# Kernel tuning notes

Hardware: AMD Instinct MI355X
Metric: run time of the kernel (lower is better)

The kernel has to match this reference:

```python
import jax, jax.numpy as jnp
from jax import lax
import numpy as np

SEQ_LEN, BATCH, INPUT_SIZE, HIDDEN_SIZE = 1024, 64, 512, 512


def setup_inputs() -> dict:
    key = jax.random.key(0)
    k1, k2, k3 = jax.random.split(key, 3)
    inputs = jax.random.normal(k1, (SEQ_LEN, BATCH, INPUT_SIZE), dtype=jnp.float32)
    # nn.Linear(input_size + hidden_size, hidden_size): W [H, I+H], b [H]
    fan_in = INPUT_SIZE + HIDDEN_SIZE
    bound = 1.0 / np.sqrt(fan_in)
    W = jax.random.uniform(k2, (HIDDEN_SIZE, fan_in), minval=-bound, maxval=bound, dtype=jnp.float32)
    b = jax.random.uniform(k3, (HIDDEN_SIZE,), minval=-bound, maxval=bound, dtype=jnp.float32)
    return {"inputs": inputs, "W": W, "b": b}


def reference(inputs, W, b):
    # inputs: [T, B, I]; hidden starts at zeros [B, H]
    hidden_size = W.shape[0]
    # Split W into hidden part and input part to avoid per-step concat:
    # layer_input = cat(h, x) -> y = h @ Wh^T + x @ Wx^T + b
    Wh = W[:, :hidden_size]          # [H, H]
    Wx = W[:, hidden_size:]          # [H, I]
    h0 = jnp.zeros((inputs.shape[1], hidden_size), dtype=inputs.dtype)

    def step(h, x):
        h_new = jnp.tanh(h @ Wh.T + x @ Wx.T + b)
        return h_new, None

    h_final, _ = lax.scan(step, h0, inputs)
    return h_final
```

## Files before the change

### kernel.cpp

```cpp
#include <hip/hip_runtime.h>


#define SEQ 1024
#define NB  64
#define HID 512

typedef _Float16 half2v __attribute__((ext_vector_type(2)));
typedef _Float16 f16x8  __attribute__((ext_vector_type(8)));
typedef float    f32x4  __attribute__((ext_vector_type(4)));

#if __has_builtin(__builtin_amdgcn_fdot2)
#define DOT2(a, b, c) __builtin_amdgcn_fdot2((a), (b), (c), false)
#else
static __device__ __forceinline__ float DOT2(half2v a, half2v b, float c) {
  return c + (float)a.x * (float)b.x + (float)a.y * (float)b.y;
}
#endif

static __device__ __forceinline__ float fast_tanh(float x) {
  float e = __expf(2.0f * x);
  return (e - 1.0f) / (e + 1.0f);
}

__global__ __launch_bounds__(256, 2)
void rnn_prepass(const float* __restrict__ X, const float* __restrict__ W,
                 const float* __restrict__ bias, _Float16* __restrict__ U) {
  __shared__ __align__(16) _Float16 As[128][40];
  __shared__ __align__(16) _Float16 Bs[128][40];
  const int tid = threadIdx.x;
  const int m0 = blockIdx.x * 128;
  const int n0 = blockIdx.y * 128;
  const int wave = tid >> 6, lane = tid & 63;
  const int wm = (wave >> 1) * 64, wn = (wave & 1) * 64;
  const int l15 = lane & 15, q = lane >> 4;

  f32x4 acc[4][4];
#pragma unroll
  for (int i = 0; i < 4; ++i)
#pragma unroll
    for (int j = 0; j < 4; ++j) acc[i][j] = (f32x4){0.f, 0.f, 0.f, 0.f};

  const int srow = tid >> 1;
  const int shalf = (tid & 1) * 16;

  for (int k0 = 0; k0 < 512; k0 += 32) {
    const float* asrc = X + (size_t)(m0 + srow) * 512 + k0 + shalf;
    const float* bsrc = W + (size_t)(n0 + srow) * 1024 + 512 + k0 + shalf;
    float4 a0 = *(const float4*)(asrc);
    float4 a1 = *(const float4*)(asrc + 4);
    float4 a2 = *(const float4*)(asrc + 8);
    float4 a3 = *(const float4*)(asrc + 12);
    float4 b0 = *(const float4*)(bsrc);
    float4 b1 = *(const float4*)(bsrc + 4);
    float4 b2 = *(const float4*)(bsrc + 8);
    float4 b3 = *(const float4*)(bsrc + 12);
    __syncthreads();
    f16x8 pa0 = {(_Float16)a0.x, (_Float16)a0.y, (_Float16)a0.z, (_Float16)a0.w,
                 (_Float16)a1.x, (_Float16)a1.y, (_Float16)a1.z, (_Float16)a1.w};
    f16x8 pa1 = {(_Float16)a2.x, (_Float16)a2.y, (_Float16)a2.z, (_Float16)a2.w,
                 (_Float16)a3.x, (_Float16)a3.y, (_Float16)a3.z, (_Float16)a3.w};
    f16x8 pb0 = {(_Float16)b0.x, (_Float16)b0.y, (_Float16)b0.z, (_Float16)b0.w,
                 (_Float16)b1.x, (_Float16)b1.y, (_Float16)b1.z, (_Float16)b1.w};
    f16x8 pb1 = {(_Float16)b2.x, (_Float16)b2.y, (_Float16)b2.z, (_Float16)b2.w,
                 (_Float16)b3.x, (_Float16)b3.y, (_Float16)b3.z, (_Float16)b3.w};
    *(f16x8*)&As[srow][shalf] = pa0;
    *(f16x8*)&As[srow][shalf + 8] = pa1;
    *(f16x8*)&Bs[srow][shalf] = pb0;
    *(f16x8*)&Bs[srow][shalf + 8] = pb1;
    __syncthreads();
    f16x8 av[4], bv[4];
#pragma unroll
    for (int i = 0; i < 4; ++i)
      av[i] = *(const f16x8*)&As[wm + i * 16 + l15][q * 8];
#pragma unroll
    for (int j = 0; j < 4; ++j)
      bv[j] = *(const f16x8*)&Bs[wn + j * 16 + l15][q * 8];
#pragma unroll
    for (int i = 0; i < 4; ++i)
#pragma unroll
      for (int j = 0; j < 4; ++j)
        acc[i][j] = __builtin_amdgcn_mfma_f32_16x16x32_f16(av[i], bv[j], acc[i][j], 0, 0, 0);
  }
  float bj[4];
#pragma unroll
  for (int j = 0; j < 4; ++j) bj[j] = bias[n0 + wn + j * 16 + l15];
#pragma unroll
  for (int i = 0; i < 4; ++i)
#pragma unroll
    for (int j = 0; j < 4; ++j)
#pragma unroll
      for (int r = 0; r < 4; ++r) {
        int m = m0 + wm + i * 16 + q * 4 + r;
        int n = n0 + wn + j * 16 + l15;
        U[(size_t)m * 512 + n] = (_Float16)(acc[i][j][r] + bj[j]);
      }
}

__global__ __launch_bounds__(256, 1)
void rnn_recur(const float* __restrict__ W, const _Float16* __restrict__ U,
               unsigned long long* hbuf, float* __restrict__ out) {
  const int blk = blockIdx.x;
  const int batch = blk & 63;
  const int g = blk >> 6;
  const int tid = threadIdx.x;
  const int rg = tid & 31;
  const int c = tid >> 5;

  __shared__ __align__(16) f16x8 wlds[32][256];
  __shared__ half2v hlds[256];
  __shared__ float part[128][9];

  {
#pragma unroll
    for (int i = 0; i < 4; ++i) {
      const float* wrow = W + (size_t)(128 * g + rg * 4 + i) * 1024 + c * 64;
#pragma unroll
      for (int qq = 0; qq < 8; ++qq) {
        float4 wa = *(const float4*)(wrow + 8 * qq);
        float4 wb = *(const float4*)(wrow + 8 * qq + 4);
        f16x8 p = {(_Float16)wa.x, (_Float16)wa.y, (_Float16)wa.z, (_Float16)wa.w,
                   (_Float16)wb.x, (_Float16)wb.y, (_Float16)wb.z, (_Float16)wb.w};
        wlds[i * 8 + qq][tid] = p;
      }
    }
  }
  __syncthreads();

  const unsigned int* ubase = (const unsigned int*)U;
  unsigned long long* hb = hbuf + (size_t)batch * 256;
  unsigned long long* hpub = hb + (size_t)(NB * 256) * 0;

  float h0f = 0.f, h1f = 0.f;
  for (int t = 0; t < SEQ; ++t) {
    unsigned int ubits = 0;
    if (tid < 64)
      ubits = ubase[((size_t)t * NB + batch) * 256 + g * 64 + tid];

    {
      const unsigned long long* src =
          hb + (size_t)(t & 1) * (NB * 256) + tid;
      unsigned long long e;
      do {
        e = __hip_atomic_load(src, __ATOMIC_RELAXED, __HIP_MEMORY_SCOPE_AGENT);
      } while ((unsigned int)(e >> 32) != (unsigned int)t);
      hlds[tid] = __builtin_bit_cast(half2v, (unsigned int)e);
    }
    __syncthreads();

    float a0 = 0.f, a1 = 0.f, a2 = 0.f, a3 = 0.f;
    const half2v* hp = &hlds[c * 32];
#pragma unroll
    for (int qq = 0; qq < 8; ++qq) {
      half2v hv0 = hp[qq * 4 + 0];
      half2v hv1 = hp[qq * 4 + 1];
      half2v hv2 = hp[qq * 4 + 2];
      half2v hv3 = hp[qq * 4 + 3];
#pragma unroll
      for (int i = 0; i < 4; ++i) {
        f16x8 wv = wlds[i * 8 + qq][tid];
        half2v w0 = {wv[0], wv[1]};
        half2v w1 = {wv[2], wv[3]};
        half2v w2 = {wv[4], wv[5]};
        half2v w3 = {wv[6], wv[7]};
        float* ai = (i == 0) ? &a0 : (i == 1) ? &a1 : (i == 2) ? &a2 : &a3;
        *ai = DOT2(w0, hv0, *ai);
        *ai = DOT2(w1, hv1, *ai);
        *ai = DOT2(w2, hv2, *ai);
        *ai = DOT2(w3, hv3, *ai);
      }
    }
    part[rg * 4 + 0][c] = a0;
    part[rg * 4 + 1][c] = a1;
    part[rg * 4 + 2][c] = a2;
    part[rg * 4 + 3][c] = a3;
    __syncthreads();

    if (tid < 64) {
      float s0 = 0.f, s1 = 0.f;
#pragma unroll
      for (int cc = 0; cc < 8; ++cc) {
        s0 += part[2 * tid][cc];
        s1 += part[2 * tid + 1][cc];
      }
      half2v uh = __builtin_bit_cast(half2v, ubits);
      h0f = fast_tanh(s0 + (float)uh.x);
      h1f = fast_tanh(s1 + (float)uh.y);
      half2v hh;
      hh.x = (_Float16)h0f;
      hh.y = (_Float16)h1f;
      unsigned long long word =
          ((unsigned long long)(unsigned int)(t + 1) << 32) |
          (unsigned long long)__builtin_bit_cast(unsigned int, hh);
      __hip_atomic_store(
          hb + (size_t)((t + 1) & 1) * (NB * 256) + g * 64 + tid, word,
          __ATOMIC_RELAXED, __HIP_MEMORY_SCOPE_AGENT);
    }
  }
  if (tid < 64) {
    out[(size_t)batch * HID + 128 * g + 2 * tid] = h0f;
    out[(size_t)batch * HID + 128 * g + 2 * tid + 1] = h1f;
  }
  (void)hpub;
}

extern "C" void kernel_launch(void* const* d_in, const int* in_sizes, int n_in,
                              void* d_out, int out_size, void* d_ws, size_t ws_size,
                              hipStream_t stream) {
  const float* X    = (const float*)d_in[0];
  const float* W    = (const float*)d_in[1];
  const float* bias = (const float*)d_in[2];
  float* out = (float*)d_out;

  char* ws = (char*)d_ws;
  _Float16* U = (_Float16*)ws;
  unsigned long long* hbuf =
      (unsigned long long*)(ws + (size_t)SEQ * NB * HID * 2);

  hipMemsetAsync(hbuf, 0, (size_t)NB * 256 * 8, stream);

  rnn_prepass<<<dim3(512, 4), dim3(256), 0, stream>>>(X, W, bias, U);

  const float* Wp = W;
  const _Float16* Up = U;
  unsigned long long* hb = hbuf;
  float* op = out;
  void* args[] = {(void*)&Wp, (void*)&Up, (void*)&hb, (void*)&op};
  hipError_t e = hipLaunchCooperativeKernel(
      reinterpret_cast<void*>(rnn_recur), dim3(256), dim3(256), args, 0, stream);
  if (e != hipSuccess) {
    rnn_recur<<<dim3(256), dim3(256), 0, stream>>>(Wp, Up, hb, op);
  }
}
```

Baseline: 1.586 ms.

## Repartition recurrent blocks to two batches by sixty-four hidden rows

The recurrent kernel now gives each block two batch rows and a 64-row slice of the hidden weight, instead of one batch and a 128-row slice. Each weight value loaded from LDS is reused for two batch columns, which halves the per-block weight LDS footprint and the weight reads per FMA. The cost is that each block must poll and load the full hidden state of two batches every step. Each step now depends on 16 producer blocks instead of 4, which can lengthen the per-step synchronisation latency.

```diff
diff --git a/kernel.cpp b/kernel.cpp
--- a/kernel.cpp
+++ b/kernel.cpp
@@ -100,87 +100,98 @@
 void rnn_recur(const float* __restrict__ W, const _Float16* __restrict__ U,
                unsigned long long* hbuf, float* __restrict__ out) {
   const int blk = blockIdx.x;
-  const int batch = blk & 63;
-  const int g = blk >> 6;
+  const int p = blk & 31;
+  const int g = blk >> 5;
   const int tid = threadIdx.x;
-  const int rg = tid & 31;
-  const int c = tid >> 5;
-
-  __shared__ __align__(16) f16x8 wlds[32][256];
-  __shared__ half2v hlds[256];
-  __shared__ float part[128][9];
-
-  {
-#pragma unroll
-    for (int i = 0; i < 4; ++i) {
-      const float* wrow = W + (size_t)(128 * g + rg * 4 + i) * 1024 + c * 64;
-#pragma unroll
-      for (int qq = 0; qq < 8; ++qq) {
-        float4 wa = *(const float4*)(wrow + 8 * qq);
-        float4 wb = *(const float4*)(wrow + 8 * qq + 4);
-        f16x8 p = {(_Float16)wa.x, (_Float16)wa.y, (_Float16)wa.z, (_Float16)wa.w,
-                   (_Float16)wb.x, (_Float16)wb.y, (_Float16)wb.z, (_Float16)wb.w};
-        wlds[i * 8 + qq][tid] = p;
-      }
-    }
-  }
-  __syncthreads();
-
-  const unsigned int* ubase = (const unsigned int*)U;
-  unsigned long long* hb = hbuf + (size_t)batch * 256;
-  unsigned long long* hpub = hb + (size_t)(NB * 256) * 0;
+  const int rb = tid & 15;
+  const int kc = tid >> 4;
+
+  __shared__ __align__(16) f16x8 wlds[16][256];
+  __shared__ __align__(16) half2v hlds[2][256];
+  __shared__ float part[128][33];
+
+#pragma unroll
+  for (int i = 0; i < 4; ++i) {
+    const float* wrow = W + (size_t)(64 * g + rb * 4 + i) * 1024 + kc * 32;
+#pragma unroll
+    for (int q = 0; q < 4; ++q) {
+      float4 wa = *(const float4*)(wrow + 8 * q);
+      float4 wb = *(const float4*)(wrow + 8 * q + 4);
+      f16x8 pk = {(_Float16)wa.x, (_Float16)wa.y, (_Float16)wa.z, (_Float16)wa.w,
+                  (_Float16)wb.x, (_Float16)wb.y, (_Float16)wb.z, (_Float16)wb.w};
+      wlds[i * 4 + q][tid] = pk;
+    }
+  }
+
+  const unsigned int* U32 = (const unsigned int*)U;
+  const int rr = tid & 31, bb = tid >> 5;
 
   float h0f = 0.f, h1f = 0.f;
   for (int t = 0; t < SEQ; ++t) {
     unsigned int ubits = 0;
     if (tid < 64)
-      ubits = ubase[((size_t)t * NB + batch) * 256 + g * 64 + tid];
+      ubits = U32[((size_t)t * 64 + 2 * p + bb) * 256 + 32 * g + rr];
 
     {
-      const unsigned long long* src =
-          hb + (size_t)(t & 1) * (NB * 256) + tid;
-      unsigned long long e;
+      const unsigned long long* s0 =
+          hbuf + (size_t)(t & 1) * (NB * 256) + (size_t)(2 * p) * 256 + tid;
+      const unsigned long long* s1 = s0 + 256;
+      unsigned long long e0 = 0, e1 = 0;
+      bool d0 = false, d1 = false;
       do {
-        e = __hip_atomic_load(src, __ATOMIC_RELAXED, __HIP_MEMORY_SCOPE_AGENT);
-      } while ((unsigned int)(e >> 32) != (unsigned int)t);
-      hlds[tid] = __builtin_bit_cast(half2v, (unsigned int)e);
-    }
-    __syncthreads();
-
-    float a0 = 0.f, a1 = 0.f, a2 = 0.f, a3 = 0.f;
-    const half2v* hp = &hlds[c * 32];
-#pragma unroll
-    for (int qq = 0; qq < 8; ++qq) {
-      half2v hv0 = hp[qq * 4 + 0];
-      half2v hv1 = hp[qq * 4 + 1];
-      half2v hv2 = hp[qq * 4 + 2];
-      half2v hv3 = hp[qq * 4 + 3];
+        if (!d0) {
+          e0 = __hip_atomic_load(s0, __ATOMIC_RELAXED, __HIP_MEMORY_SCOPE_AGENT);
+          d0 = ((unsigned int)(e0 >> 32) == (unsigned int)t);
+        }
+        if (!d1) {
+          e1 = __hip_atomic_load(s1, __ATOMIC_RELAXED, __HIP_MEMORY_SCOPE_AGENT);
+          d1 = ((unsigned int)(e1 >> 32) == (unsigned int)t);
+        }
+      } while (!(d0 && d1));
+      hlds[0][tid] = __builtin_bit_cast(half2v, (unsigned int)e0);
+      hlds[1][tid] = __builtin_bit_cast(half2v, (unsigned int)e1);
+    }
+    __syncthreads();
+
+    float a00 = 0.f, a01 = 0.f, a02 = 0.f, a03 = 0.f;
+    float a10 = 0.f, a11 = 0.f, a12 = 0.f, a13 = 0.f;
+#pragma unroll
+    for (int q = 0; q < 4; ++q) {
+      f16x8 h8a = *(const f16x8*)&hlds[0][kc * 16 + q * 4];
+      f16x8 h8b = *(const f16x8*)&hlds[1][kc * 16 + q * 4];
+      half2v ha0 = {h8a[0], h8a[1]}, ha1 = {h8a[2], h8a[3]};
+      half2v ha2 = {h8a[4], h8a[5]}, ha3 = {h8a[6], h8a[7]};
+      half2v hb0 = {h8b[0], h8b[1]}, hb1 = {h8b[2], h8b[3]};
+      half2v hb2 = {h8b[4], h8b[5]}, hb3 = {h8b[6], h8b[7]};
 #pragma unroll
       for (int i = 0; i < 4; ++i) {
-        f16x8 wv = wlds[i * 8 + qq][tid];
-        half2v w0 = {wv[0], wv[1]};
-        half2v w1 = {wv[2], wv[3]};
-        half2v w2 = {wv[4], wv[5]};
-        half2v w3 = {wv[6], wv[7]};
-        float* ai = (i == 0) ? &a0 : (i == 1) ? &a1 : (i == 2) ? &a2 : &a3;
-        *ai = DOT2(w0, hv0, *ai);
-        *ai = DOT2(w1, hv1, *ai);
-        *ai = DOT2(w2, hv2, *ai);
-        *ai = DOT2(w3, hv3, *ai);
+        f16x8 wv = wlds[i * 4 + q][tid];
+        half2v w0 = {wv[0], wv[1]}, w1 = {wv[2], wv[3]};
+        half2v w2 = {wv[4], wv[5]}, w3 = {wv[6], wv[7]};
+        float* pa = (i == 0) ? &a00 : (i == 1) ? &a01 : (i == 2) ? &a02 : &a03;
+        float* pb = (i == 0) ? &a10 : (i == 1) ? &a11 : (i == 2) ? &a12 : &a13;
+        *pa = DOT2(w0, ha0, *pa); *pa = DOT2(w1, ha1, *pa);
+        *pa = DOT2(w2, ha2, *pa); *pa = DOT2(w3, ha3, *pa);
+        *pb = DOT2(w0, hb0, *pb); *pb = DOT2(w1, hb1, *pb);
+        *pb = DOT2(w2, hb2, *pb); *pb = DOT2(w3, hb3, *pb);
       }
     }
-    part[rg * 4 + 0][c] = a0;
-    part[rg * 4 + 1][c] = a1;
-    part[rg * 4 + 2][c] = a2;
-    part[rg * 4 + 3][c] = a3;
+    part[rb * 4 + 0][kc] = a00;
+    part[rb * 4 + 1][kc] = a01;
+    part[rb * 4 + 2][kc] = a02;
+    part[rb * 4 + 3][kc] = a03;
+    part[64 + rb * 4 + 0][kc] = a10;
+    part[64 + rb * 4 + 1][kc] = a11;
+    part[64 + rb * 4 + 2][kc] = a12;
+    part[64 + rb * 4 + 3][kc] = a13;
     __syncthreads();
 
     if (tid < 64) {
       float s0 = 0.f, s1 = 0.f;
 #pragma unroll
-      for (int cc = 0; cc < 8; ++cc) {
-        s0 += part[2 * tid][cc];
-        s1 += part[2 * tid + 1][cc];
+      for (int kk = 0; kk < 16; ++kk) {
+        s0 += part[bb * 64 + 2 * rr][kk];
+        s1 += part[bb * 64 + 2 * rr + 1][kk];
       }
       half2v uh = __builtin_bit_cast(half2v, ubits);
       h0f = fast_tanh(s0 + (float)uh.x);
@@ -192,15 +203,15 @@
           ((unsigned long long)(unsigned int)(t + 1) << 32) |
           (unsigned long long)__builtin_bit_cast(unsigned int, hh);
       __hip_atomic_store(
-          hb + (size_t)((t + 1) & 1) * (NB * 256) + g * 64 + tid, word,
-          __ATOMIC_RELAXED, __HIP_MEMORY_SCOPE_AGENT);
+          hbuf + (size_t)((t + 1) & 1) * (NB * 256) +
+              (size_t)(2 * p + bb) * 256 + 32 * g + rr,
+          word, __ATOMIC_RELAXED, __HIP_MEMORY_SCOPE_AGENT);
     }
   }
   if (tid < 64) {
-    out[(size_t)batch * HID + 128 * g + 2 * tid] = h0f;
-    out[(size_t)batch * HID + 128 * g + 2 * tid + 1] = h1f;
-  }
-  (void)hpub;
+    out[(size_t)(2 * p + bb) * HID + 64 * g + 2 * rr]     = h0f;
+    out[(size_t)(2 * p + bb) * HID + 64 * g + 2 * rr + 1] = h1f;
+  }
 }
 
 extern "C" void kernel_launch(void* const* d_in, const int* in_sizes, int n_in,
```

After: 2.106 ms. 32.8% more time.

## Replace LDS partial-sum reduction with wave shuffles and double-buffer hidden state

Applied to the files above, without the earlier changes.

Each group of 8 consecutive lanes now splits the K dimension for four output rows, and the partial sums are combined with xor shuffles instead of a shared-memory partial array. This removes one __syncthreads per timestep. The hidden-state LDS buffer is double-buffered so the next step's writes cannot clobber reads from the current step, and the spin loop adds s_sleep backoff. Each lane now publishes two packed words, and the initial barrier after the weight load is gone; correctness relies on the first in-loop barrier.

```diff
diff --git a/kernel.cpp b/kernel.cpp
--- a/kernel.cpp
+++ b/kernel.cpp
@@ -103,104 +103,94 @@
   const int batch = blk & 63;
   const int g = blk >> 6;
   const int tid = threadIdx.x;
-  const int rg = tid & 31;
-  const int c = tid >> 5;
-
-  __shared__ __align__(16) f16x8 wlds[32][256];
-  __shared__ half2v hlds[256];
-  __shared__ float part[128][9];
-
-  {
-#pragma unroll
-    for (int i = 0; i < 4; ++i) {
-      const float* wrow = W + (size_t)(128 * g + rg * 4 + i) * 1024 + c * 64;
-#pragma unroll
-      for (int qq = 0; qq < 8; ++qq) {
-        float4 wa = *(const float4*)(wrow + 8 * qq);
-        float4 wb = *(const float4*)(wrow + 8 * qq + 4);
-        f16x8 p = {(_Float16)wa.x, (_Float16)wa.y, (_Float16)wa.z, (_Float16)wa.w,
-                   (_Float16)wb.x, (_Float16)wb.y, (_Float16)wb.z, (_Float16)wb.w};
-        wlds[i * 8 + qq][tid] = p;
+  const int ks = tid & 7;
+  const int rg = tid >> 3;
+
+  __shared__ __align__(16) f16x8 wl[32][256];
+  __shared__ __align__(16) half2v hlds[2][256];
+
+#pragma unroll
+  for (int i = 0; i < 4; ++i) {
+    const float* wrow = W + (size_t)(128 * g + 4 * rg + i) * 1024 + ks * 64;
+#pragma unroll
+    for (int q = 0; q < 8; ++q) {
+      float4 wa = *(const float4*)(wrow + 8 * q);
+      float4 wb = *(const float4*)(wrow + 8 * q + 4);
+      f16x8 pk = {(_Float16)wa.x, (_Float16)wa.y, (_Float16)wa.z, (_Float16)wa.w,
+                  (_Float16)wb.x, (_Float16)wb.y, (_Float16)wb.z, (_Float16)wb.w};
+      wl[i * 8 + q][tid] = pk;
+    }
+  }
+
+  const unsigned long long* U64 = (const unsigned long long*)U;
+  unsigned long long* hb = hbuf + (size_t)batch * 256;
+
+  float hv0 = 0.f, hv1 = 0.f, hv2 = 0.f, hv3 = 0.f;
+  for (int t = 0; t < SEQ; ++t) {
+    unsigned long long uld = 0;
+    if (ks == 0)
+      uld = U64[(((size_t)t * NB + batch) * HID + 128 * g + 4 * rg) >> 2];
+
+    {
+      const unsigned long long* src = hb + (size_t)(t & 1) * (NB * 256) + tid;
+      unsigned long long e;
+      int spins = 0;
+      for (;;) {
+        e = __hip_atomic_load(src, __ATOMIC_RELAXED, __HIP_MEMORY_SCOPE_AGENT);
+        if ((unsigned int)(e >> 32) == (unsigned int)t) break;
+        if (++spins > 2) __builtin_amdgcn_s_sleep(1);
       }
-    }
-  }
-  __syncthreads();
-
-  const unsigned int* ubase = (const unsigned int*)U;
-  unsigned long long* hb = hbuf + (size_t)batch * 256;
-  unsigned long long* hpub = hb + (size_t)(NB * 256) * 0;
-
-  float h0f = 0.f, h1f = 0.f;
-  for (int t = 0; t < SEQ; ++t) {
-    unsigned int ubits = 0;
-    if (tid < 64)
-      ubits = ubase[((size_t)t * NB + batch) * 256 + g * 64 + tid];
-
-    {
-      const unsigned long long* src =
-          hb + (size_t)(t & 1) * (NB * 256) + tid;
-      unsigned long long e;
-      do {
-        e = __hip_atomic_load(src, __ATOMIC_RELAXED, __HIP_MEMORY_SCOPE_AGENT);
-      } while ((unsigned int)(e >> 32) != (unsigned int)t);
-      hlds[tid] = __builtin_bit_cast(half2v, (unsigned int)e);
+      hlds[t & 1][tid] = __builtin_bit_cast(half2v, (unsigned int)e);
     }
     __syncthreads();
 
     float a0 = 0.f, a1 = 0.f, a2 = 0.f, a3 = 0.f;
-    const half2v* hp = &hlds[c * 32];
-#pragma unroll
-    for (int qq = 0; qq < 8; ++qq) {
-      half2v hv0 = hp[qq * 4 + 0];
-      half2v hv1 = hp[qq * 4 + 1];
-      half2v hv2 = hp[qq * 4 + 2];
-      half2v hv3 = hp[qq * 4 + 3];
+    const half2v* hp = &hlds[t & 1][ks * 32];
+#pragma unroll
+    for (int q = 0; q < 8; ++q) {
+      f16x8 h8 = *(const f16x8*)&hp[q * 4];
+      half2v h0 = {h8[0], h8[1]}, h1 = {h8[2], h8[3]};
+      half2v h2 = {h8[4], h8[5]}, h3 = {h8[6], h8[7]};
 #pragma unroll
       for (int i = 0; i < 4; ++i) {
-        f16x8 wv = wlds[i * 8 + qq][tid];
-        half2v w0 = {wv[0], wv[1]};
-        half2v w1 = {wv[2], wv[3]};
-        half2v w2 = {wv[4], wv[5]};
-        half2v w3 = {wv[6], wv[7]};
+        f16x8 wv = wl[i * 8 + q][tid];
+        half2v w0 = {wv[0], wv[1]}, w1 = {wv[2], wv[3]};
+        half2v w2 = {wv[4], wv[5]}, w3 = {wv[6], wv[7]};
         float* ai = (i == 0) ? &a0 : (i == 1) ? &a1 : (i == 2) ? &a2 : &a3;
-        *ai = DOT2(w0, hv0, *ai);
-        *ai = DOT2(w1, hv1, *ai);
-        *ai = DOT2(w2, hv2, *ai);
-        *ai = DOT2(w3, hv3, *ai);
+        *ai = DOT2(w0, h0, *ai); *ai = DOT2(w1, h1, *ai);
+        *ai = DOT2(w2, h2, *ai); *ai = DOT2(w3, h3, *ai);
       }
     }
-    part[rg * 4 + 0][c] = a0;
-    part[rg * 4 + 1][c] = a1;
-    part[rg * 4 + 2][c] = a2;
-    part[rg * 4 + 3][c] = a3;
-    __syncthreads();
-
-    if (tid < 64) {
-      float s0 = 0.f, s1 = 0.f;
-#pragma unroll
-      for (int cc = 0; cc < 8; ++cc) {
-        s0 += part[2 * tid][cc];
-        s1 += part[2 * tid + 1][cc];
-      }
-      half2v uh = __builtin_bit_cast(half2v, ubits);
-      h0f = fast_tanh(s0 + (float)uh.x);
-      h1f = fast_tanh(s1 + (float)uh.y);
-      half2v hh;
-      hh.x = (_Float16)h0f;
-      hh.y = (_Float16)h1f;
-      unsigned long long word =
-          ((unsigned long long)(unsigned int)(t + 1) << 32) |
-          (unsigned long long)__builtin_bit_cast(unsigned int, hh);
-      __hip_atomic_store(
-          hb + (size_t)((t + 1) & 1) * (NB * 256) + g * 64 + tid, word,
-          __ATOMIC_RELAXED, __HIP_MEMORY_SCOPE_AGENT);
-    }
-  }
-  if (tid < 64) {
-    out[(size_t)batch * HID + 128 * g + 2 * tid] = h0f;
-    out[(size_t)batch * HID + 128 * g + 2 * tid + 1] = h1f;
-  }
-  (void)hpub;
+#pragma unroll
+    for (int m = 1; m < 8; m <<= 1) {
+      a0 += __shfl_xor(a0, m);
+      a1 += __shfl_xor(a1, m);
+      a2 += __shfl_xor(a2, m);
+      a3 += __shfl_xor(a3, m);
+    }
+
+    if (ks == 0) {
+      f16x8 u8;
+      *(unsigned long long*)&u8 = uld;
+      hv0 = fast_tanh(a0 + (float)u8[0]);
+      hv1 = fast_tanh(a1 + (float)u8[1]);
+      hv2 = fast_tanh(a2 + (float)u8[2]);
+      hv3 = fast_tanh(a3 + (float)u8[3]);
+      half2v p01; p01.x = (_Float16)hv0; p01.y = (_Float16)hv1;
+      half2v p23; p23.x = (_Float16)hv2; p23.y = (_Float16)hv3;
+      unsigned long long tg = (unsigned long long)(unsigned int)(t + 1) << 32;
+      unsigned long long w01 = tg | __builtin_bit_cast(unsigned int, p01);
+      unsigned long long w23 = tg | __builtin_bit_cast(unsigned int, p23);
+      unsigned long long* dst =
+          hb + (size_t)((t + 1) & 1) * (NB * 256) + 64 * g + 2 * rg;
+      __hip_atomic_store(dst, w01, __ATOMIC_RELAXED, __HIP_MEMORY_SCOPE_AGENT);
+      __hip_atomic_store(dst + 1, w23, __ATOMIC_RELAXED, __HIP_MEMORY_SCOPE_AGENT);
+    }
+  }
+  if (ks == 0) {
+    float* o = out + (size_t)batch * HID + 128 * g + 4 * rg;
+    o[0] = hv0; o[1] = hv1; o[2] = hv2; o[3] = hv3;
+  }
 }
 
 extern "C" void kernel_launch(void* const* d_in, const int* in_sizes, int n_in,
```

After: 2.176 ms. 1.37x slower.
